# Performance work log

Measured on AMD Instinct MI355X. Metric: run time of the kernel, lower is better.

Reference implementation:

```python
import jax, jax.numpy as jnp
import numpy as np

NV, NE = 4096, 8192
FV, FE = 128, 64
FV_OUT = 128


def setup_inputs() -> dict:
    key = jax.random.key(0)
    ks = jax.random.split(key, 8)
    stdv = 1.0 / np.sqrt(FV_OUT)
    return {
        "H_v": jax.random.normal(ks[0], (NV, FV), dtype=jnp.float32),
        "H_e": jax.random.normal(ks[1], (NE, FE), dtype=jnp.float32),
        "adj_e": jax.random.uniform(ks[2], (NE, NE), dtype=jnp.float32),
        "adj_v": jax.random.uniform(ks[3], (NV, NV), dtype=jnp.float32),
        "T": jax.random.uniform(ks[4], (NV, NE), dtype=jnp.float32),
        "weight": jax.random.uniform(ks[5], (FV, FV_OUT), minval=-stdv, maxval=stdv, dtype=jnp.float32),
        "p": jax.random.normal(ks[6], (1, FE), dtype=jnp.float32),
        "bias": jax.random.uniform(ks[7], (FV_OUT,), minval=-stdv, maxval=stdv, dtype=jnp.float32),
    }


def reference(H_v, H_e, adj_e, adj_v, T, weight, p, bias):
    # node_layer=True path of GraphConvolution.forward
    # d = (H_e @ p.T) as a vector over edges; T @ diag(d) == T * d[None, :]
    d = (H_e @ p.T)[:, 0]                       # [Ne]
    multiplier = (T * d[None, :]) @ T.T         # [Nv, Nv]
    n = multiplier.shape[0]
    mask = jnp.eye(n, dtype=multiplier.dtype)   # eye mask: diag -> 1, off-diag -> multiplier
    M1 = mask + (1.0 - mask) * multiplier
    adjusted_A = M1 * adj_v                     # elementwise mask with dense adjacency
    output = adjusted_A @ (H_v @ weight) + bias # [Nv, Fv_out]
    return (output, H_e)
```

## Files before the change

kernel.cpp:

```cpp
#include <hip/hip_runtime.h>
#include <stdint.h>

#define NV 4096
#define NE 8192
#define FV 128
#define FE 64
#define FOUT 128

typedef unsigned short u16;
typedef __attribute__((ext_vector_type(8))) short short8;
typedef __attribute__((ext_vector_type(4))) float f32x4;
typedef __attribute__((ext_vector_type(4))) unsigned short u16x4;

__device__ __forceinline__ u16 f2bf(float f) {
  uint32_t u = __builtin_bit_cast(uint32_t, f);
  u += 0x7fffu + ((u >> 16) & 1u);
  return (u16)(u >> 16);
}

#define AS1(p) ((__attribute__((address_space(1))) void*)(void*)(p))
#define AS3(p) ((__attribute__((address_space(3))) void*)(p))

__global__ __launch_bounds__(64) void k_edge_dot(const float* __restrict__ He,
                                                 const float* __restrict__ p,
                                                 float* __restrict__ d) {
  int e = blockIdx.x;
  int l = threadIdx.x;
  float v = He[e * FE + l] * p[l];
  #pragma unroll
  for (int off = 32; off > 0; off >>= 1) v += __shfl_down(v, off);
  if (l == 0) d[e] = v;
}

__global__ __launch_bounds__(256) void k_convert(const float* __restrict__ T,
                                                 const float* __restrict__ d,
                                                 u16* __restrict__ Ta,
                                                 u16* __restrict__ Tb) {
  size_t idx = ((size_t)blockIdx.x * 256 + threadIdx.x) * 4;
  f32x4 t = *(const f32x4*)&T[idx];
  int e = (int)(idx & (NE - 1));
  f32x4 dv = *(const f32x4*)&d[e];
  u16x4 a, b;
  a.x = f2bf(t.x * dv.x); a.y = f2bf(t.y * dv.y);
  a.z = f2bf(t.z * dv.z); a.w = f2bf(t.w * dv.w);
  b.x = f2bf(t.x); b.y = f2bf(t.y); b.z = f2bf(t.z); b.w = f2bf(t.w);
  *(u16x4*)&Ta[idx] = a;
  *(u16x4*)&Tb[idx] = b;
}

__global__ __launch_bounds__(128) void k_hw(const float* __restrict__ Hv,
                                            const float* __restrict__ W,
                                            u16* __restrict__ HWt) {
  __shared__ float sh[FV];
  int i = blockIdx.x;
  int n = threadIdx.x;
  sh[n] = Hv[i * FV + n];
  __syncthreads();
  float s = 0.f;
  #pragma unroll
  for (int f = 0; f < FV; ++f) s += sh[f] * W[f * FOUT + n];
  HWt[(size_t)n * NV + i] = f2bf(s);
}

__global__ __launch_bounds__(256) void k_init_out(float* __restrict__ out,
                                                  const float* __restrict__ bias,
                                                  const float* __restrict__ He) {
  int idx = blockIdx.x * 256 + threadIdx.x;
  if (idx < NV * FOUT) out[idx] = bias[idx & (FOUT - 1)];
  else out[idx] = He[idx - NV * FOUT];
}

__global__ __launch_bounds__(256) void k_gemm_mult(const u16* __restrict__ Ta,
                                                   const u16* __restrict__ Tb,
                                                   const float* __restrict__ adjv,
                                                   u16* __restrict__ adjA) {
  __shared__ __align__(16) u16 lA[128 * 32];
  __shared__ __align__(16) u16 lB[128 * 32];
  const int K = NE;
  const int tile_m = blockIdx.y * 128;
  const int tile_n = blockIdx.x * 128;
  const int tid = threadIdx.x;
  const int lane = tid & 63;
  const int wave = tid >> 6;
  const int wm = (wave >> 1) * 64;
  const int wn = (wave & 1) * 64;
  const int row16 = lane & 15;
  const int quad = lane >> 4;

  f32x4 acc[4][4] = {};

  for (int k0 = 0; k0 < K; k0 += 32) {
    __syncthreads();
    #pragma unroll
    for (int r = 0; r < 2; ++r) {
      const int chunk = r * 256 + wave * 64 + lane;
      const int row = chunk >> 2;
      const int cc = chunk & 3;
      const u16* ga = Ta + ((size_t)(tile_m + row) * K + k0 + cc * 8);
      const u16* gb = Tb + ((size_t)(tile_n + row) * K + k0 + cc * 8);
      __builtin_amdgcn_global_load_lds(AS1(ga), AS3(&lA[(r * 256 + wave * 64) * 8]), 16, 0, 0);
      __builtin_amdgcn_global_load_lds(AS1(gb), AS3(&lB[(r * 256 + wave * 64) * 8]), 16, 0, 0);
    }
    __syncthreads();
    short8 a[4], b[4];
    #pragma unroll
    for (int mi = 0; mi < 4; ++mi)
      a[mi] = *(const short8*)&lA[(wm + mi * 16 + row16) * 32 + quad * 8];
    #pragma unroll
    for (int ni = 0; ni < 4; ++ni)
      b[ni] = *(const short8*)&lB[(wn + ni * 16 + row16) * 32 + quad * 8];
    #pragma unroll
    for (int mi = 0; mi < 4; ++mi)
      #pragma unroll
      for (int ni = 0; ni < 4; ++ni)
        acc[mi][ni] = __builtin_amdgcn_mfma_f32_16x16x32_bf16(a[mi], b[ni], acc[mi][ni], 0, 0, 0);
  }

  #pragma unroll
  for (int mi = 0; mi < 4; ++mi) {
    #pragma unroll
    for (int ni = 0; ni < 4; ++ni) {
      const int gc = tile_n + wn + ni * 16 + row16;
      #pragma unroll
      for (int r = 0; r < 4; ++r) {
        const int gr = tile_m + wm + mi * 16 + quad * 4 + r;
        float v = acc[mi][ni][r];
        if (gr == gc) v = 1.0f;
        v *= adjv[(size_t)gr * NV + gc];
        adjA[(size_t)gr * NV + gc] = f2bf(v);
      }
    }
  }
}

#define KSPLIT 8
__global__ __launch_bounds__(256) void k_gemm_out(const u16* __restrict__ A,
                                                  const u16* __restrict__ B,
                                                  float* __restrict__ out) {
  __shared__ __align__(16) u16 lA[128 * 32];
  __shared__ __align__(16) u16 lB[128 * 32];
  const int K = NV;
  const int tile_m = blockIdx.y * 128;
  const int kbeg = blockIdx.x * (K / KSPLIT);
  const int kend = kbeg + (K / KSPLIT);
  const int tid = threadIdx.x;
  const int lane = tid & 63;
  const int wave = tid >> 6;
  const int wm = (wave >> 1) * 64;
  const int wn = (wave & 1) * 64;
  const int row16 = lane & 15;
  const int quad = lane >> 4;

  f32x4 acc[4][4] = {};

  for (int k0 = kbeg; k0 < kend; k0 += 32) {
    __syncthreads();
    #pragma unroll
    for (int r = 0; r < 2; ++r) {
      const int chunk = r * 256 + wave * 64 + lane;
      const int row = chunk >> 2;
      const int cc = chunk & 3;
      const u16* ga = A + ((size_t)(tile_m + row) * K + k0 + cc * 8);
      const u16* gb = B + ((size_t)row * K + k0 + cc * 8);
      __builtin_amdgcn_global_load_lds(AS1(ga), AS3(&lA[(r * 256 + wave * 64) * 8]), 16, 0, 0);
      __builtin_amdgcn_global_load_lds(AS1(gb), AS3(&lB[(r * 256 + wave * 64) * 8]), 16, 0, 0);
    }
    __syncthreads();
    short8 a[4], b[4];
    #pragma unroll
    for (int mi = 0; mi < 4; ++mi)
      a[mi] = *(const short8*)&lA[(wm + mi * 16 + row16) * 32 + quad * 8];
    #pragma unroll
    for (int ni = 0; ni < 4; ++ni)
      b[ni] = *(const short8*)&lB[(wn + ni * 16 + row16) * 32 + quad * 8];
    #pragma unroll
    for (int mi = 0; mi < 4; ++mi)
      #pragma unroll
      for (int ni = 0; ni < 4; ++ni)
        acc[mi][ni] = __builtin_amdgcn_mfma_f32_16x16x32_bf16(a[mi], b[ni], acc[mi][ni], 0, 0, 0);
  }

  #pragma unroll
  for (int mi = 0; mi < 4; ++mi) {
    #pragma unroll
    for (int ni = 0; ni < 4; ++ni) {
      const int gc = wn + ni * 16 + row16;
      #pragma unroll
      for (int r = 0; r < 4; ++r) {
        const int gr = tile_m + wm + mi * 16 + quad * 4 + r;
        atomicAdd(&out[(size_t)gr * FOUT + gc], acc[mi][ni][r]);
      }
    }
  }
}

extern "C" void kernel_launch(void* const* d_in, const int* in_sizes, int n_in,
                              void* d_out, int out_size, void* d_ws, size_t ws_size,
                              hipStream_t stream) {
  const float* Hv   = (const float*)d_in[0];
  const float* He   = (const float*)d_in[1];
  const float* adjv = (const float*)d_in[3];
  const float* T    = (const float*)d_in[4];
  const float* W    = (const float*)d_in[5];
  const float* p    = (const float*)d_in[6];
  const float* bias = (const float*)d_in[7];
  float* out = (float*)d_out;

  char* ws = (char*)d_ws;
  float* dvec = (float*)ws;
  u16* HWt  = (u16*)(ws + ((size_t)1 << 20));
  u16* Ta   = (u16*)(ws + ((size_t)2 << 20));
  u16* Tb   = (u16*)(ws + ((size_t)2 << 20) + ((size_t)64 << 20));
  u16* adjA = (u16*)(ws + ((size_t)2 << 20) + ((size_t)128 << 20));

  k_edge_dot<<<NE, 64, 0, stream>>>(He, p, dvec);
  k_convert<<<(NV * NE) / (256 * 4), 256, 0, stream>>>(T, dvec, Ta, Tb);
  k_hw<<<NV, 128, 0, stream>>>(Hv, W, HWt);
  k_init_out<<<(NV * FOUT + NE * FE) / 256, 256, 0, stream>>>(out, bias, He);
  k_gemm_mult<<<dim3(NV / 128, NV / 128), 256, 0, stream>>>(Ta, Tb, adjv, adjA);
  k_gemm_out<<<dim3(KSPLIT, NV / 128), 256, 0, stream>>>(adjA, HWt, out);
}
```

Measured before the change: 827.2 us.

## Exploit symmetry of T·diag(d)·Tᵀ to compute only lower-triangle tiles

The multiplier matrix is symmetric, so the GEMM now launches only lower-triangular 128x128 tiles and writes each off-diagonal tile a second time, transposed through LDS, with its own adjacency mask applied. This roughly halves the FLOPs of the dominant K=8192 GEMM. The cost is an extra LDS transpose, a second masked store, and uneven work per tile. The split-K factor of the output GEMM is also raised to add parallelism, at the price of more atomics.

```diff
diff --git a/kernel.cpp b/kernel.cpp
--- a/kernel.cpp
+++ b/kernel.cpp
@@ -16,6 +16,9 @@
   uint32_t u = __builtin_bit_cast(uint32_t, f);
   u += 0x7fffu + ((u >> 16) & 1u);
   return (u16)(u >> 16);
+}
+__device__ __forceinline__ float bf2f(u16 h) {
+  return __builtin_bit_cast(float, (uint32_t)h << 16);
 }
 
 #define AS1(p) ((__attribute__((address_space(1))) void*)(void*)(p))
@@ -74,11 +77,20 @@
                                                    const u16* __restrict__ Tb,
                                                    const float* __restrict__ adjv,
                                                    u16* __restrict__ adjA) {
-  __shared__ __align__(16) u16 lA[128 * 32];
-  __shared__ __align__(16) u16 lB[128 * 32];
+  __shared__ __align__(16) u16 smem[128 * 136];
+  u16* lA = smem;
+  u16* lB = smem + 4096;
+  u16* sT = smem;
+
+  int id = blockIdx.x;
+  int bi = (int)((sqrtf(8.0f * (float)id + 1.0f) - 1.0f) * 0.5f);
+  while ((bi + 1) * (bi + 2) / 2 <= id) ++bi;
+  while (bi * (bi + 1) / 2 > id) --bi;
+  int bj = id - bi * (bi + 1) / 2;
+
   const int K = NE;
-  const int tile_m = blockIdx.y * 128;
-  const int tile_n = blockIdx.x * 128;
+  const int tile_m = bi * 128;
+  const int tile_n = bj * 128;
   const int tid = threadIdx.x;
   const int lane = tid & 63;
   const int wave = tid >> 6;
@@ -131,9 +143,41 @@
       }
     }
   }
-}
-
-#define KSPLIT 8
+
+  if (bi != bj) {
+    __syncthreads();
+    #pragma unroll
+    for (int mi = 0; mi < 4; ++mi) {
+      #pragma unroll
+      for (int ni = 0; ni < 4; ++ni) {
+        const int c = wn + ni * 16 + row16;
+        const int r0 = wm + mi * 16 + quad * 4;
+        u16x4 pk;
+        pk.x = f2bf(acc[mi][ni][0]); pk.y = f2bf(acc[mi][ni][1]);
+        pk.z = f2bf(acc[mi][ni][2]); pk.w = f2bf(acc[mi][ni][3]);
+        *(u16x4*)&sT[c * 136 + r0] = pk;
+      }
+    }
+    __syncthreads();
+    const int row = tid >> 1;
+    const int half = tid & 1;
+    const size_t obase = (size_t)(tile_n + row) * NV + tile_m + half * 64;
+    const u16* srow = &sT[row * 136 + half * 64];
+    #pragma unroll
+    for (int j = 0; j < 8; ++j) {
+      short8 m8 = *(const short8*)&srow[j * 8];
+      short8 o8;
+      #pragma unroll
+      for (int k = 0; k < 8; ++k) {
+        float v = bf2f((u16)m8[k]) * adjv[obase + j * 8 + k];
+        o8[k] = (short)f2bf(v);
+      }
+      *(short8*)&adjA[obase + j * 8] = o8;
+    }
+  }
+}
+
+#define KSPLIT 16
 __global__ __launch_bounds__(256) void k_gemm_out(const u16* __restrict__ A,
                                                   const u16* __restrict__ B,
                                                   float* __restrict__ out) {
@@ -217,6 +261,6 @@
   k_convert<<<(NV * NE) / (256 * 4), 256, 0, stream>>>(T, dvec, Ta, Tb);
   k_hw<<<NV, 128, 0, stream>>>(Hv, W, HWt);
   k_init_out<<<(NV * FOUT + NE * FE) / 256, 256, 0, stream>>>(out, bias, He);
-  k_gemm_mult<<<dim3(NV / 128, NV / 128), 256, 0, stream>>>(Ta, Tb, adjv, adjA);
+  k_gemm_mult<<<(32 * 33) / 2, 256, 0, stream>>>(Ta, Tb, adjv, adjA);
   k_gemm_out<<<dim3(KSPLIT, NV / 128), 256, 0, stream>>>(adjA, HWt, out);
 }
```

New measurement: 827.7 us. Within noise of the previous version (+0.1%).
